# Kernel optimization log

Hardware: AMD Instinct MI355X
Metric: run time of the kernel (lower is better)

## Reference

```python
import jax, jax.numpy as jnp
import numpy as np
from jax import lax

D_MODEL = 1024
D_STATE = 128
D_CONV = 4
EXPAND = 2
HEADDIM = 64
D_INNER = EXPAND * D_MODEL          # 2048
NHEADS = D_INNER // HEADDIM         # 32
D_IN_PROJ = 2 * D_INNER + 2 * D_STATE + NHEADS  # 4384 (z, xBC, dt)
CONV_CH = D_INNER + 2 * D_STATE     # 2304
CHUNK = 128
EPS = 1e-5
BATCH, SEQ = 2, 2048


def silu(x):
    return x * jax.nn.sigmoid(x)


def rmsnorm(x, w):
    return x * lax.rsqrt(jnp.mean(x * x, axis=-1, keepdims=True) + EPS) * w


def segsum(a):
    # a: (b,h,c,q) -> (b,h,c,q,q); [i,j] = sum_{j<k<=i} a_k, -inf above diag
    q = a.shape[-1]
    cs = jnp.cumsum(a, axis=-1)
    seg = cs[..., :, None] - cs[..., None, :]
    mask = jnp.tril(jnp.ones((q, q), dtype=bool))
    return jnp.where(mask, seg, -jnp.inf)


def ssd(xh, dt, A, B, C):
    # xh: (b,l,h,p), dt: (b,l,h), A: (h,), B,C: (b,l,n). Chunked SSD scan.
    b, l, h, p = xh.shape
    n = B.shape[-1]
    c = l // CHUNK
    X = (xh * dt[..., None]).reshape(b, c, CHUNK, h, p)
    Adt = (A * dt).reshape(b, c, CHUNK, h).transpose(0, 3, 1, 2)  # (b,h,c,q)
    Bc = B.reshape(b, c, CHUNK, n)
    Cc = C.reshape(b, c, CHUNK, n)
    Acs = jnp.cumsum(Adt, axis=-1)
    L = jnp.exp(segsum(Adt))  # (b,h,c,q,q) causal decay within chunk
    Y_diag = jnp.einsum('bcln,bcsn,bhcls,bcshp->bclhp', Cc, Bc, L, X)
    decay_states = jnp.exp(Acs[..., -1:] - Acs)
    states = jnp.einsum('bcln,bhcl,bclhp->bchpn', Bc, decay_states, X)
    chunk_decay = jnp.exp(Acs[..., -1])  # (b,h,c)

    def step(s, inp):
        st, cd = inp
        return s * cd[:, :, None, None] + st, s

    init = jnp.zeros((b, h, p, n), dtype=xh.dtype)
    _, prev = lax.scan(step, init,
                       (states.transpose(1, 0, 2, 3, 4), chunk_decay.transpose(2, 0, 1)))
    # prev: (c,b,h,p,n) = state at start of each chunk
    Y_off = jnp.einsum('bcln,cbhpn,bhcl->bclhp', Cc, prev, jnp.exp(Acs))
    return (Y_diag + Y_off).reshape(b, l, h, p)


def mamba2(x, in_w, conv_w, conv_b, dt_bias, A_log, D, gnorm_w, out_w):
    b, l, _ = x.shape
    zxbcdt = x @ in_w.T  # (b,l,D_IN_PROJ)
    z = zxbcdt[..., :D_INNER]
    xBC = zxbcdt[..., D_INNER:D_INNER + CONV_CH]
    dt = jax.nn.softplus(zxbcdt[..., D_INNER + CONV_CH:] + dt_bias)  # (b,l,h)
    # causal depthwise conv1d
    xp = jnp.pad(xBC, ((0, 0), (D_CONV - 1, 0), (0, 0)))
    conv = sum(xp[:, k:k + l, :] * conv_w[:, k] for k in range(D_CONV)) + conv_b
    xBC = silu(conv)
    xs = xBC[..., :D_INNER]
    B = xBC[..., D_INNER:D_INNER + D_STATE]
    C = xBC[..., D_INNER + D_STATE:]
    A = -jnp.exp(A_log)
    xh = xs.reshape(b, l, NHEADS, HEADDIM)
    y = ssd(xh, dt, A, B, C) + xh * D[None, None, :, None]
    y = y.reshape(b, l, D_INNER)
    y = rmsnorm(y * silu(z), gnorm_w)  # RMSNormGated
    return y @ out_w.T


def setup_inputs() -> dict:
    key = jax.random.key(0)
    ks = jax.random.split(key, 24)
    d = {}
    d['x'] = jax.random.normal(ks[0], (BATCH, SEQ, D_MODEL), dtype=jnp.float32)
    d['norm_w'] = jnp.ones((D_MODEL,), jnp.float32)
    d['out_w_blk'] = jax.random.normal(ks[1], (D_MODEL, 2 * D_MODEL), jnp.float32) * 0.02
    d['out_b_blk'] = jnp.zeros((D_MODEL,), jnp.float32)
    for i, pfx in enumerate(['f_', 'b_']):
        o = 2 + i * 10
        d[pfx + 'in_w'] = jax.random.normal(ks[o], (D_IN_PROJ, D_MODEL), jnp.float32) * 0.02
        d[pfx + 'conv_w'] = jax.random.normal(ks[o + 1], (CONV_CH, D_CONV), jnp.float32) * 0.2
        d[pfx + 'conv_b'] = jnp.zeros((CONV_CH,), jnp.float32)
        d[pfx + 'dt_bias'] = jax.random.normal(ks[o + 2], (NHEADS,), jnp.float32) * 0.1
        d[pfx + 'A_log'] = jnp.log(jax.random.uniform(ks[o + 3], (NHEADS,), jnp.float32, 1.0, 16.0))
        d[pfx + 'D'] = jnp.ones((NHEADS,), jnp.float32)
        d[pfx + 'gnorm_w'] = jnp.ones((D_INNER,), jnp.float32)
        d[pfx + 'out_w'] = jax.random.normal(ks[o + 4], (D_MODEL, D_INNER), jnp.float32) * 0.02
    return d


def reference(x, norm_w, out_w_blk, out_b_blk,
              f_in_w, f_conv_w, f_conv_b, f_dt_bias, f_A_log, f_D, f_gnorm_w, f_out_w,
              b_in_w, b_conv_w, b_conv_b, b_dt_bias, b_A_log, b_D, b_gnorm_w, b_out_w):
    xn = rmsnorm(x, norm_w)
    y_fwd = mamba2(xn, f_in_w, f_conv_w, f_conv_b, f_dt_bias, f_A_log, f_D, f_gnorm_w, f_out_w)
    y_bwd = jnp.flip(
        mamba2(jnp.flip(xn, axis=1), b_in_w, b_conv_w, b_conv_b, b_dt_bias, b_A_log, b_D, b_gnorm_w, b_out_w),
        axis=1)
    out = jnp.concatenate([y_fwd, y_bwd], axis=-1) @ out_w_blk.T + out_b_blk
    return x + out
```

## Files before the change

kernel.cpp:

```cpp
#include <hip/hip_runtime.h>
#include <hip/hip_bf16.h>
#include <math.h>

#define BATCH 2
#define SEQL 2048
#define T 4096
#define DMODEL 1024
#define DINNER 2048
#define DSTATE 128
#define NH 32
#define HD 64
#define DPROJ2 4352
#define CONVCH 2304
#define NCH 16
#define CHUNK 128
#define EPS 1e-5f

#define N_INW ((size_t)DPROJ2 * DMODEL)
#define N_OUTW ((size_t)DMODEL * DINNER)
#define N_ST ((size_t)BATCH * NCH * NH * HD * DSTATE)
#define F2B_BLOCKS 10752
#define TW_BLOCKS 1024

typedef unsigned short u16;
typedef __bf16 bf16x8 __attribute__((ext_vector_type(8)));
typedef float f32x4 __attribute__((ext_vector_type(4)));

__device__ __forceinline__ u16 f2b(float f) {
    union { float f; unsigned u; } v; v.f = f;
    unsigned r = v.u + 0x7fffu + ((v.u >> 16) & 1u);
    return (u16)(r >> 16);
}
__device__ __forceinline__ float b2f(u16 b) {
    union { unsigned u; float f; } v; v.u = ((unsigned)b) << 16;
    return v.f;
}
__device__ __forceinline__ int flipseq(int r) {
    return (r & ~(SEQL - 1)) | ((SEQL - 1) - (r & (SEQL - 1)));
}
__device__ __forceinline__ void gload16(const u16* g, u16* l) {
    __builtin_amdgcn_global_load_lds(
        (const __attribute__((address_space(1))) void*)g,
        (__attribute__((address_space(3))) void*)l, 16, 0, 0);
}

#define FENCE asm volatile("" ::: "memory")

__device__ __forceinline__ float blockReduceSum(float v) {
    __shared__ float red_[4];
    for (int off = 32; off > 0; off >>= 1) v += __shfl_down(v, off);
    int lane = threadIdx.x & 63, wid = threadIdx.x >> 6;
    if (lane == 0) red_[wid] = v;
    __syncthreads();
    if (threadIdx.x == 0) {
        float s = 0.f;
        int nw = blockDim.x >> 6;
        for (int i = 0; i < nw; ++i) s += red_[i];
        red_[0] = s;
    }
    __syncthreads();
    return red_[0];
}

__global__ __launch_bounds__(256) void k_rmsdt(
    const float* __restrict__ x, const float* __restrict__ w,
    const float* __restrict__ inw_f, const float* __restrict__ inw_b,
    const float* __restrict__ dtb_f, const float* __restrict__ dtb_b,
    u16* __restrict__ outb, float* __restrict__ dt)
{
    __shared__ float xs[4][1024];
    int r0 = blockIdx.x * 4;
    int tid = threadIdx.x;
    int lane = tid & 63, wv = tid >> 6;
    int row = r0 + wv;
    const float* xr = x + (size_t)row * DMODEL;
    float4 v[4];
    float ss = 0.f;
    #pragma unroll
    for (int i = 0; i < 4; ++i) {
        v[i] = *(const float4*)(xr + (i * 64 + lane) * 4);
        ss += v[i].x * v[i].x + v[i].y * v[i].y + v[i].z * v[i].z + v[i].w * v[i].w;
    }
    #pragma unroll
    for (int off = 32; off > 0; off >>= 1) ss += __shfl_down(ss, off);
    ss = __shfl(ss, 0);
    float sc = rsqrtf(ss / DMODEL + EPS);
    #pragma unroll
    for (int i = 0; i < 4; ++i) {
        int c = (i * 64 + lane) * 4;
        float4 wv4 = *(const float4*)(w + c);
        ushort4 o;
        o.x = f2b(v[i].x * sc * wv4.x);
        o.y = f2b(v[i].y * sc * wv4.y);
        o.z = f2b(v[i].z * sc * wv4.z);
        o.w = f2b(v[i].w * sc * wv4.w);
        *(ushort4*)(outb + (size_t)row * DMODEL + c) = o;
        xs[wv][c + 0] = b2f(o.x); xs[wv][c + 1] = b2f(o.y);
        xs[wv][c + 2] = b2f(o.z); xs[wv][c + 3] = b2f(o.w);
    }
    __syncthreads();
    int h2 = tid >> 2, part = tid & 3;
    int dir = h2 >> 5, h = h2 & 31;
    const float* wd = (dir ? inw_b : inw_f) + (size_t)(DPROJ2 + h) * DMODEL;
    float a0 = 0.f, a1 = 0.f, a2 = 0.f, a3 = 0.f;
    for (int kk = 0; kk < 256; ++kk) {
        int k = part + (kk << 2);
        float wvv = wd[k];
        a0 += xs[0][k] * wvv; a1 += xs[1][k] * wvv;
        a2 += xs[2][k] * wvv; a3 += xs[3][k] * wvv;
    }
    #pragma unroll
    for (int off = 2; off > 0; off >>= 1) {
        a0 += __shfl_down(a0, off, 4); a1 += __shfl_down(a1, off, 4);
        a2 += __shfl_down(a2, off, 4); a3 += __shfl_down(a3, off, 4);
    }
    if (part == 0) {
        float bsh = dir ? dtb_b[h] : dtb_f[h];
        float* dtp = dt + (size_t)dir * T * NH;
        float vv[4] = {a0, a1, a2, a3};
        #pragma unroll
        for (int rr = 0; rr < 4; ++rr) {
            int rg = r0 + rr;
            if (dir) rg = flipseq(rg);
            float vvv = vv[rr] + bsh;
            dtp[(size_t)rg * NH + h] = (vvv > 20.f) ? vvv : log1pf(expf(vvv));
        }
    }
}

__global__ __launch_bounds__(256) void k_wprep(
    const float* __restrict__ f_in_w, const float* __restrict__ b_in_w,
    const float* __restrict__ out_w_blk,
    const float* __restrict__ f_out_w, const float* __restrict__ b_out_w,
    u16* __restrict__ d_inwb, u16* __restrict__ d_owbb, u16* __restrict__ d_fowT)
{
    __shared__ u16 t[64][65];
    int bid = blockIdx.x;
    if (bid < F2B_BLOCKS) {
        size_t i = ((size_t)bid * 256 + threadIdx.x) * 4;
        const float* s; u16* d; size_t off;
        if (i < 2 * N_INW) {
            int dir = i >= N_INW;
            off = i - (size_t)dir * N_INW;
            s = dir ? b_in_w : f_in_w; d = d_inwb + (size_t)dir * N_INW;
        } else {
            off = i - 2 * N_INW;
            if (off >= N_OUTW) return;
            s = out_w_blk; d = d_owbb;
        }
        float4 v = *(const float4*)(s + off);
        ushort4 o;
        o.x = f2b(v.x); o.y = f2b(v.y); o.z = f2b(v.z); o.w = f2b(v.w);
        *(ushort4*)(d + off) = o;
        return;
    }
    int b2 = bid - F2B_BLOCKS;
    int dir = b2 >> 9;
    int rem = b2 & 511;
    int c0 = (rem & 31) * 64, e0 = (rem >> 5) * 64;
    const float* src = dir ? b_out_w : f_out_w;
    u16* d = d_fowT + (size_t)dir * N_OUTW;
    for (int i = threadIdx.x; i < 64 * 16; i += 256) {
        int el = i >> 4, c4 = (i & 15) * 4;
        float4 v = *(const float4*)(src + (size_t)(e0 + el) * DINNER + c0 + c4);
        t[c4 + 0][el] = f2b(v.x); t[c4 + 1][el] = f2b(v.y);
        t[c4 + 2][el] = f2b(v.z); t[c4 + 3][el] = f2b(v.w);
    }
    __syncthreads();
    for (int i = threadIdx.x; i < 64 * 16; i += 256) {
        int cl = i >> 4, e4 = (i & 15) * 4;
        ushort4 o;
        o.x = t[cl][e4]; o.y = t[cl][e4 + 1]; o.z = t[cl][e4 + 2]; o.w = t[cl][e4 + 3];
        *(ushort4*)(d + (size_t)(c0 + cl) * DMODEL + e0 + e4) = o;
    }
}

__global__ __launch_bounds__(512, 2) void k_mm_in8(
    const u16* __restrict__ A, const u16* __restrict__ W0,
    u16* __restrict__ zb0, u16* __restrict__ xbcraw0)
{
    __shared__ u16 lds_[8 * 8192];
    int dir = blockIdx.z;
    const u16* W = W0 + (size_t)dir * N_INW;

    int f = blockIdx.x + (blockIdx.y << 4);
    int xcd = f & 7;
    int jj = f >> 3;
    int m0 = (jj >> 1) * 256;
    int n0 = ((xcd << 1) | (jj & 1)) * 256;

    u16* Cout; int ldcc, nbase;
    if (n0 < DINNER) {
        Cout = zb0 + (size_t)dir * T * DINNER;
        ldcc = DINNER;
        nbase = n0;
    } else {
        Cout = xbcraw0 + (size_t)dir * T * CONVCH;
        ldcc = CONVCH;
        nbase = n0 - DINNER;
    }

    int tid = threadIdx.x;
    int lane = tid & 63;
    int w = tid >> 6;
    int wm = w >> 2;
    int wn = w & 3;
    int l15 = lane & 15;
    int gsw0 = (((lane >> 4) ^ (lane & 7)) << 3);
    int gsw1 = (((4 + (lane >> 4)) ^ (lane & 7)) << 3);

    const u16* pA[2][2];
    const u16* pB[2][2];
    int swz = ((lane & 7) ^ (lane >> 3)) << 3;
    #pragma unroll
    for (int h = 0; h < 2; ++h)
        #pragma unroll
        for (int c = 0; c < 2; ++c) {
            int rl = (w * 2 + c) * 8 + (lane >> 3);
            int grow = m0 + h * 128 + rl;
            if (dir) grow = flipseq(grow);
            pA[h][c] = A + (size_t)grow * DMODEL + swz;
            pB[h][c] = W + (size_t)(n0 + h * 128 + rl) * DMODEL + swz;
        }
    int dst0 = (w * 2 + 0) * 512 + lane * 8;
    int dst1 = (w * 2 + 1) * 512 + lane * 8;

#define STAGE_A(t_, h_) do { \
        gload16(pA[h_][0] + (t_) * 64, lds_ + (((t_) & 1) * 4 + (h_)) * 8192 + dst0); \
        gload16(pA[h_][1] + (t_) * 64, lds_ + (((t_) & 1) * 4 + (h_)) * 8192 + dst1); \
    } while (0)
#define STAGE_B(t_, h_) do { \
        gload16(pB[h_][0] + (t_) * 64, lds_ + (((t_) & 1) * 4 + 2 + (h_)) * 8192 + dst0); \
        gload16(pB[h_][1] + (t_) * 64, lds_ + (((t_) & 1) * 4 + 2 + (h_)) * 8192 + dst1); \
    } while (0)

    f32x4 acc[8][4] = {};
    bf16x8 bfv[4][2];

    STAGE_A(0, 0); STAGE_A(0, 1); STAGE_B(0, 0); STAGE_B(0, 1);
    FENCE;
    STAGE_B(1, 0); STAGE_B(1, 1);
    asm volatile("s_waitcnt vmcnt(4)" ::: "memory");
    __builtin_amdgcn_s_barrier();
    FENCE;

    for (int kt = 0; kt < 16; ++kt) {
        int d = kt & 1;
        const u16* Ab = lds_ + (d * 4 + wm) * 8192;
        const u16* Bb = lds_ + (d * 4 + 2 + (wn >> 1)) * 8192;
        int nrow0 = (wn & 1) * 64;
        #pragma unroll
        for (int q = 0; q < 4; ++q) {
            if (q == 0) {
                #pragma unroll
                for (int j = 0; j < 4; ++j) {
                    const u16* bp = Bb + (nrow0 + j * 16 + l15) * 64;
                    bfv[j][0] = *(const bf16x8*)(bp + gsw0);
                    bfv[j][1] = *(const bf16x8*)(bp + gsw1);
                }
            }
            const u16* ap0 = Ab + ((q * 2 + 0) * 16 + l15) * 64;
            const u16* ap1 = Ab + ((q * 2 + 1) * 16 + l15) * 64;
            bf16x8 a0k0 = *(const bf16x8*)(ap0 + gsw0);
            bf16x8 a0k1 = *(const bf16x8*)(ap0 + gsw1);
            bf16x8 a1k0 = *(const bf16x8*)(ap1 + gsw0);
            bf16x8 a1k1 = *(const bf16x8*)(ap1 + gsw1);
            if (q == 0)      { if (kt < 15) STAGE_A(kt + 1, 0); }
            else if (q == 1) { if (kt < 15) STAGE_A(kt + 1, 1); }
            else if (q == 2) { if (kt < 14) STAGE_B(kt + 2, 0); }
            else             { if (kt < 14) STAGE_B(kt + 2, 1); }
            FENCE;
            __builtin_amdgcn_s_barrier();
            asm volatile("s_waitcnt lgkmcnt(0)" ::: "memory");
            __builtin_amdgcn_s_setprio(1);
            #pragma unroll
            for (int j = 0; j < 4; ++j) {
                acc[q * 2 + 0][j] = __builtin_amdgcn_mfma_f32_16x16x32_bf16(a0k0, bfv[j][0], acc[q * 2 + 0][j], 0, 0, 0);
                acc[q * 2 + 0][j] = __builtin_amdgcn_mfma_f32_16x16x32_bf16(a0k1, bfv[j][1], acc[q * 2 + 0][j], 0, 0, 0);
                acc[q * 2 + 1][j] = __builtin_amdgcn_mfma_f32_16x16x32_bf16(a1k0, bfv[j][0], acc[q * 2 + 1][j], 0, 0, 0);
                acc[q * 2 + 1][j] = __builtin_amdgcn_mfma_f32_16x16x32_bf16(a1k1, bfv[j][1], acc[q * 2 + 1][j], 0, 0, 0);
            }
            __builtin_amdgcn_s_setprio(0);
            if (q == 3) {
                if (kt < 14)       asm volatile("s_waitcnt vmcnt(4)" ::: "memory");
                else if (kt == 14) asm volatile("s_waitcnt vmcnt(0)" ::: "memory");
            }
            FENCE;
            __builtin_amdgcn_s_barrier();
            FENCE;
        }
    }
#undef STAGE_A
#undef STAGE_B

    int rb = m0 + wm * 128 + ((lane >> 4) << 2);
    int cb = nbase + wn * 64 + l15;
    #pragma unroll
    for (int i = 0; i < 8; ++i)
        #pragma unroll
        for (int j = 0; j < 4; ++j)
            #pragma unroll
            for (int r = 0; r < 4; ++r)
                Cout[(size_t)(rb + i * 16 + r) * ldcc + cb + j * 16] = f2b(acc[i][j][r]);
}

__global__ __launch_bounds__(256, 4) void k_mm_in(
    const u16* __restrict__ A, const u16* __restrict__ W0,
    u16* __restrict__ zb0, u16* __restrict__ xbcraw0, int ny0)
{
    const int K = DMODEL;
    int dir = blockIdx.z;
    const u16* W = W0 + (size_t)dir * N_INW;
    int m0 = blockIdx.x * 128, n0 = (blockIdx.y + ny0) * 128;

    u16* Cout;
    int ldcc, nbase;
    if (n0 < DINNER) {
        Cout = zb0 + (size_t)dir * T * DINNER;
        ldcc = DINNER;
        nbase = n0;
    } else {
        Cout = xbcraw0 + (size_t)dir * T * CONVCH;
        ldcc = CONVCH;
        nbase = n0 - DINNER;
    }

    __shared__ u16 As[2 * 128 * 32];
    __shared__ u16 Bs[2 * 128 * 32];
    int tid = threadIdx.x;
    int lane = tid & 63;
    int wrow = ((tid >> 6) & 1) * 64, wcol = (tid >> 7) * 64;

    int srow = tid >> 2, skof = (tid & 3) * 8;
    int ar1 = m0 + srow, ar2 = ar1 + 64;
    if (dir) { ar1 = flipseq(ar1); ar2 = flipseq(ar2); }
    const u16* ga1 = A + (size_t)ar1 * K + skof;
    const u16* ga2 = A + (size_t)ar2 * K + skof;
    const u16* gb1 = W + (size_t)(n0 + srow) * K + skof;
    const u16* gb2 = gb1 + (size_t)64 * K;
    u16* la1 = As + tid * 8;
    u16* la2 = As + 2048 + tid * 8;
    u16* lb1 = Bs + tid * 8;
    u16* lb2 = Bs + 2048 + tid * 8;

    int aoff[4], boff[4];
    #pragma unroll
    for (int i = 0; i < 4; ++i) {
        aoff[i] = (wrow + i * 16 + (lane & 15)) * 32 + ((lane >> 4) * 8);
        boff[i] = (wcol + i * 16 + (lane & 15)) * 32 + ((lane >> 4) * 8);
    }

    f32x4 acc[4][4] = {};
    for (int kt = 0; kt < K; kt += 64) {
        gload16(ga1, la1);        gload16(ga2, la2);
        gload16(ga1 + 32, la1 + 4096); gload16(ga2 + 32, la2 + 4096);
        gload16(gb1, lb1);        gload16(gb2, lb2);
        gload16(gb1 + 32, lb1 + 4096); gload16(gb2 + 32, lb2 + 4096);
        ga1 += 64; ga2 += 64; gb1 += 64; gb2 += 64;
        __syncthreads();
        #pragma unroll
        for (int ks = 0; ks < 2; ++ks) {
            bf16x8 af[4], bfv[4];
            #pragma unroll
            for (int i = 0; i < 4; ++i) af[i] = *(const bf16x8*)(As + ks * 4096 + aoff[i]);
            #pragma unroll
            for (int j = 0; j < 4; ++j) bfv[j] = *(const bf16x8*)(Bs + ks * 4096 + boff[j]);
            #pragma unroll
            for (int i = 0; i < 4; ++i)
                #pragma unroll
                for (int j = 0; j < 4; ++j)
                    acc[i][j] = __builtin_amdgcn_mfma_f32_16x16x32_bf16(af[i], bfv[j], acc[i][j], 0, 0, 0);
        }
        __syncthreads();
    }

    int rbase = m0 + wrow + ((lane >> 4) << 2);
    int cbase = nbase + wcol + (lane & 15);
    #pragma unroll
    for (int i = 0; i < 4; ++i)
        #pragma unroll
        for (int j = 0; j < 4; ++j)
            #pragma unroll
            for (int r = 0; r < 4; ++r)
                Cout[(size_t)(rbase + i * 16 + r) * ldcc + cbase + j * 16] = f2b(acc[i][j][r]);
}

__global__ __launch_bounds__(256) void k_mm64(
    const u16* __restrict__ A0, const u16* __restrict__ W0,
    u16* __restrict__ Cb)
{
    int dir = blockIdx.z;
    const u16* A = A0 + dir * DMODEL;
    const u16* W = W0 + (size_t)dir * N_OUTW;

    __shared__ u16 As[2 * 128 * 32];
    __shared__ u16 Bs[2 * 64 * 32];
    int tid = threadIdx.x;
    int lane = tid & 63;
    int w = tid >> 6;
    int m0 = blockIdx.y * 128, n0 = blockIdx.x * 64;
    int wrow = (w & 1) * 64, wcol = (w >> 1) * 32;

    int srow = tid >> 2, skof = (tid & 3) * 8;
    const u16* ga1 = A + (size_t)(m0 + srow) * 2048 + skof;
    const u16* ga2 = A + (size_t)(m0 + 64 + srow) * 2048 + skof;
    const u16* gb  = W + (size_t)(n0 + srow) * DMODEL + skof;
    u16* la1 = As + tid * 8;
    u16* la2 = As + 2048 + tid * 8;
    u16* lb  = Bs + tid * 8;

    int aoff[4], boff[2];
    #pragma unroll
    for (int i = 0; i < 4; ++i)
        aoff[i] = (wrow + i * 16 + (lane & 15)) * 32 + ((lane >> 4) * 8);
    #pragma unroll
    for (int j = 0; j < 2; ++j)
        boff[j] = (wcol + j * 16 + (lane & 15)) * 32 + ((lane >> 4) * 8);

    f32x4 acc[4][2] = {};
    for (int kt = 0; kt < DMODEL; kt += 64) {
        gload16(ga1, la1); gload16(ga1 + 32, la1 + 4096);
        gload16(ga2, la2); gload16(ga2 + 32, la2 + 4096);
        gload16(gb, lb);   gload16(gb + 32, lb + 2048);
        ga1 += 64; ga2 += 64; gb += 64;
        __syncthreads();
        #pragma unroll
        for (int ks = 0; ks < 2; ++ks) {
            bf16x8 af[4], bfv[2];
            #pragma unroll
            for (int i = 0; i < 4; ++i) af[i] = *(const bf16x8*)(As + ks * 4096 + aoff[i]);
            #pragma unroll
            for (int j = 0; j < 2; ++j) bfv[j] = *(const bf16x8*)(Bs + ks * 2048 + boff[j]);
            #pragma unroll
            for (int i = 0; i < 4; ++i)
                #pragma unroll
                for (int j = 0; j < 2; ++j)
                    acc[i][j] = __builtin_amdgcn_mfma_f32_16x16x32_bf16(af[i], bfv[j], acc[i][j], 0, 0, 0);
        }
        __syncthreads();
    }

    int rbase = m0 + wrow + ((lane >> 4) << 2);
    int cbase = n0 + wcol + (lane & 15);
    #pragma unroll
    for (int i = 0; i < 4; ++i)
        #pragma unroll
        for (int j = 0; j < 2; ++j)
            #pragma unroll
            for (int r = 0; r < 4; ++r)
                Cb[(size_t)(rbase + i * 16 + r) * 4096 + dir * 2048 + cbase + j * 16] = f2b(acc[i][j][r]);
}

__global__ __launch_bounds__(256) void k_mm_fin(
    const u16* __restrict__ A1, const u16* __restrict__ A2,
    const u16* __restrict__ W,
    float* __restrict__ out, const float* __restrict__ bias,
    const float* __restrict__ resid)
{
    __shared__ u16 As[4 * 128 * 32];
    __shared__ u16 Bs[2 * 2 * 64 * 32];
    int tid = threadIdx.x;
    int lane = tid & 63;
    int w = tid >> 6;
    int m0 = blockIdx.y * 128, n0 = blockIdx.x * 64;
    int wrow = (w & 1) * 64, wcol = (w >> 1) * 32;

    int srow = tid >> 2, skof = (tid & 3) * 8;
    const u16* ga1  = A1 + (size_t)(m0 + srow) * DINNER + skof;
    const u16* ga1b = A1 + (size_t)(m0 + 64 + srow) * DINNER + skof;
    const u16* ga2  = A2 + (size_t)flipseq(m0 + srow) * DINNER + skof;
    const u16* ga2b = A2 + (size_t)flipseq(m0 + 64 + srow) * DINNER + skof;
    const u16* gb1 = W + (size_t)(n0 + srow) * 4096 + skof;
    const u16* gb2 = gb1 + 2048;
    u16* la1  = As + tid * 8;
    u16* la1b = As + 2048 + tid * 8;
    u16* la2  = As + 8192 + tid * 8;
    u16* la2b = As + 8192 + 2048 + tid * 8;
    u16* lb1 = Bs + tid * 8;
    u16* lb2 = Bs + 4096 + tid * 8;

    int aoff[4], boff[2];
    #pragma unroll
    for (int i = 0; i < 4; ++i)
        aoff[i] = (wrow + i * 16 + (lane & 15)) * 32 + ((lane >> 4) * 8);
    #pragma unroll
    for (int j = 0; j < 2; ++j)
        boff[j] = (wcol + j * 16 + (lane & 15)) * 32 + ((lane >> 4) * 8);

    f32x4 acc[4][2] = {};
    for (int kt = 0; kt < DINNER; kt += 64) {
        gload16(ga1, la1);    gload16(ga1 + 32, la1 + 4096);
        gload16(ga1b, la1b);  gload16(ga1b + 32, la1b + 4096);
        gload16(ga2, la2);    gload16(ga2 + 32, la2 + 4096);
        gload16(ga2b, la2b);  gload16(ga2b + 32, la2b + 4096);
        gload16(gb1, lb1);    gload16(gb1 + 32, lb1 + 2048);
        gload16(gb2, lb2);    gload16(gb2 + 32, lb2 + 2048);
        ga1 += 64; ga1b += 64; ga2 += 64; ga2b += 64; gb1 += 64; gb2 += 64;
        __syncthreads();
        #pragma unroll
        for (int h = 0; h < 2; ++h) {
            #pragma unroll
            for (int ks = 0; ks < 2; ++ks) {
                bf16x8 af[4], bfv[2];
                #pragma unroll
                for (int i = 0; i < 4; ++i)
                    af[i] = *(const bf16x8*)(As + h * 8192 + ks * 4096 + aoff[i]);
                #pragma unroll
                for (int j = 0; j < 2; ++j)
                    bfv[j] = *(const bf16x8*)(Bs + h * 4096 + ks * 2048 + boff[j]);
                #pragma unroll
                for (int i = 0; i < 4; ++i)
                    #pragma unroll
                    for (int j = 0; j < 2; ++j)
                        acc[i][j] = __builtin_amdgcn_mfma_f32_16x16x32_bf16(af[i], bfv[j], acc[i][j], 0, 0, 0);
            }
        }
        __syncthreads();
    }

    int rbase = m0 + wrow + ((lane >> 4) << 2);
    int cbase = n0 + wcol + (lane & 15);
    #pragma unroll
    for (int i = 0; i < 4; ++i)
        #pragma unroll
        for (int j = 0; j < 2; ++j)
            #pragma unroll
            for (int r = 0; r < 4; ++r) {
                int row = rbase + i * 16 + r, col = cbase + j * 16;
                out[(size_t)row * DMODEL + col] =
                    acc[i][j][r] + bias[col] + resid[(size_t)row * DMODEL + col];
            }
}

__global__ void k_conv(const u16* __restrict__ xraw0,
                       const float* __restrict__ cw_f, const float* __restrict__ cw_b,
                       const float* __restrict__ cb_f, const float* __restrict__ cb_b,
                       const float* __restrict__ dt0,
                       u16* __restrict__ xbcb0, u16* __restrict__ xdtb0)
{
    int dir = blockIdx.z;
    const u16* xraw = xraw0 + (size_t)dir * T * CONVCH;
    const float* cw = dir ? cw_b : cw_f;
    const float* cb = dir ? cb_b : cb_f;
    const float* dt = dt0 + (size_t)dir * T * NH;
    u16* xbcb = xbcb0 + (size_t)dir * T * CONVCH;
    u16* xdtb = xdtb0 + (size_t)dir * T * DINNER;

    int idx = blockIdx.x * blockDim.x + threadIdx.x;
    if (idx >= (T / 4) * (CONVCH / 8)) return;
    int r4 = idx / (CONVCH / 8);
    int c8 = (idx - r4 * (CONVCH / 8)) * 8;
    int r0 = r4 * 4;
    int t0 = r0 & (SEQL - 1);

    float4 cwv[8];
    #pragma unroll
    for (int j = 0; j < 8; ++j) cwv[j] = *(const float4*)(cw + (size_t)(c8 + j) * 4);
    float acc[4][8];
    {
        float4 c0 = *(const float4*)(cb + c8);
        float4 c1 = *(const float4*)(cb + c8 + 4);
        #pragma unroll
        for (int i = 0; i < 4; ++i) {
            acc[i][0] = c0.x; acc[i][1] = c0.y; acc[i][2] = c0.z; acc[i][3] = c0.w;
            acc[i][4] = c1.x; acc[i][5] = c1.y; acc[i][6] = c1.z; acc[i][7] = c1.w;
        }
    }
    #pragma unroll
    for (int s = 0; s < 7; ++s) {
        int tt = t0 - 3 + s;
        if (tt < 0) continue;
        const u16* src = xraw + (size_t)(r0 - 3 + s) * CONVCH + c8;
        ushort4 v0 = *(const ushort4*)src;
        ushort4 v1 = *(const ushort4*)(src + 4);
        float xv[8] = {b2f(v0.x), b2f(v0.y), b2f(v0.z), b2f(v0.w),
                       b2f(v1.x), b2f(v1.y), b2f(v1.z), b2f(v1.w)};
        #pragma unroll
        for (int i = 0; i < 4; ++i) {
            if (i <= s && i >= s - 3) {
                const int j = s - i;
                #pragma unroll
                for (int ch = 0; ch < 8; ++ch) {
                    float wv = (j == 0) ? cwv[ch].x : (j == 1) ? cwv[ch].y
                             : (j == 2) ? cwv[ch].z : cwv[ch].w;
                    acc[i][ch] += xv[ch] * wv;
                }
            }
        }
    }
    #pragma unroll
    for (int i = 0; i < 4; ++i) {
        int r = r0 + i;
        float sgl[8];
        #pragma unroll
        for (int ch = 0; ch < 8; ++ch) sgl[ch] = acc[i][ch] / (1.f + __expf(-acc[i][ch]));
        ushort4 o0, o1;
        o0.x = f2b(sgl[0]); o0.y = f2b(sgl[1]); o0.z = f2b(sgl[2]); o0.w = f2b(sgl[3]);
        o1.x = f2b(sgl[4]); o1.y = f2b(sgl[5]); o1.z = f2b(sgl[6]); o1.w = f2b(sgl[7]);
        *(ushort4*)(xbcb + (size_t)r * CONVCH + c8) = o0;
        *(ushort4*)(xbcb + (size_t)r * CONVCH + c8 + 4) = o1;
        if (c8 < DINNER) {
            float dv = dt[(size_t)r * NH + (c8 >> 6)];
            ushort4 d0, d1;
            d0.x = f2b(sgl[0] * dv); d0.y = f2b(sgl[1] * dv);
            d0.z = f2b(sgl[2] * dv); d0.w = f2b(sgl[3] * dv);
            d1.x = f2b(sgl[4] * dv); d1.y = f2b(sgl[5] * dv);
            d1.z = f2b(sgl[6] * dv); d1.w = f2b(sgl[7] * dv);
            *(ushort4*)(xdtb + (size_t)r * DINNER + c8) = d0;
            *(ushort4*)(xdtb + (size_t)r * DINNER + c8 + 4) = d1;
        }
    }
}

#define LDW 136
__global__ __launch_bounds__(256) void k_states(
    const u16* __restrict__ xbcb0, const u16* __restrict__ xdtb0,
    const float* __restrict__ dt0,
// ... 164 lines not shown
    for (int i = 0; i < 4; ++i)
        #pragma unroll
        for (int j = 0; j < 4; ++j) {
            int s = wcol + j * 16 + (lane & 15);
            #pragma unroll
            for (int r = 0; r < 4; ++r) {
                int l = wrow + i * 16 + (lane >> 4) * 4 + r;
                float v = (s <= l) ? sacc[i][j][r] * __expf(acs_s[l] - acs_s[s]) : 0.f;
                S0[l * LDW + s] = f2b(v);
            }
        }
    __syncthreads();
    f32x4 yacc[2][4] = {};
    for (int kk = 0; kk < 4; ++kk) {
        bf16x8 af[2], bfr[4];
        #pragma unroll
        for (int i = 0; i < 2; ++i)
            af[i] = *(const bf16x8*)(S0 + (w * 32 + i * 16 + (lane & 15)) * LDW
                                     + kk * 32 + (lane >> 4) * 8);
        #pragma unroll
        for (int j = 0; j < 4; ++j)
            bfr[j] = *(const bf16x8*)(Xt + (j * 16 + (lane & 15)) * LDW
                                      + kk * 32 + (lane >> 4) * 8);
        #pragma unroll
        for (int i = 0; i < 2; ++i)
            #pragma unroll
            for (int j = 0; j < 4; ++j)
                yacc[i][j] = __builtin_amdgcn_mfma_f32_16x16x32_bf16(af[i], bfr[j], yacc[i][j], 0, 0, 0);
    }
    __syncthreads();
    size_t sb = (size_t)blockIdx.x * (HD * DSTATE);
    for (int i = tid; i < 64 * 16; i += 256) {
        int p = i >> 4, m8 = (i & 15) * 8;
        *(uint4*)(S0 + p * LDW + m8) = *(const uint4*)(prev + sb + (size_t)p * DSTATE + m8);
    }
    __syncthreads();
    f32x4 oacc[2][4] = {};
    for (int kk = 0; kk < 4; ++kk) {
        bf16x8 af[2], bfr[4];
        #pragma unroll
        for (int i = 0; i < 2; ++i)
            af[i] = *(const bf16x8*)(cbase + (size_t)(w * 32 + i * 16 + (lane & 15)) * CONVCH
                                     + kk * 32 + (lane >> 4) * 8);
        #pragma unroll
        for (int j = 0; j < 4; ++j)
            bfr[j] = *(const bf16x8*)(S0 + (j * 16 + (lane & 15)) * LDW
                                      + kk * 32 + (lane >> 4) * 8);
        #pragma unroll
        for (int i = 0; i < 2; ++i)
            #pragma unroll
            for (int j = 0; j < 4; ++j)
                oacc[i][j] = __builtin_amdgcn_mfma_f32_16x16x32_bf16(af[i], bfr[j], oacc[i][j], 0, 0, 0);
    }
    float Dh = Dp[h];
    #pragma unroll
    for (int i = 0; i < 2; ++i)
        #pragma unroll
        for (int j = 0; j < 4; ++j)
            #pragma unroll
            for (int r = 0; r < 4; ++r) {
                int l = w * 32 + i * 16 + (lane >> 4) * 4 + r;
                int p = j * 16 + (lane & 15);
                float val = yacc[i][j][r] + __expf(acs_s[l]) * oacc[i][j][r]
                          + b2f(xbcb[(size_t)(row0 + l) * CONVCH + h * HD + p]) * Dh;
                y[(size_t)(row0 + l) * DINNER + h * HD + p] = f2b(val);
            }
}

__global__ __launch_bounds__(256) void k_gate(
    const u16* __restrict__ y0, const u16* __restrict__ zb0,
    const float* __restrict__ gw_f, const float* __restrict__ gw_b,
    u16* __restrict__ out0)
{
    int dir = blockIdx.z;
    const u16* y = y0 + (size_t)dir * T * DINNER;
    const u16* zb = zb0 + (size_t)dir * T * DINNER;
    const float* gw = dir ? gw_b : gw_f;
    u16* out = out0 + (size_t)dir * T * DINNER;

    int r = blockIdx.x;
    int tid = threadIdx.x;
    float tv[8];
    float ss = 0.f;
    #pragma unroll
    for (int it = 0; it < 2; ++it) {
        int i = (it * 256 + tid) * 4;
        ushort4 yv = *(const ushort4*)(y + (size_t)r * DINNER + i);
        ushort4 zv = *(const ushort4*)(zb + (size_t)r * DINNER + i);
        float z0 = b2f(zv.x), z1 = b2f(zv.y), z2 = b2f(zv.z), z3 = b2f(zv.w);
        float t0 = b2f(yv.x) * (z0 / (1.f + __expf(-z0)));
        float t1 = b2f(yv.y) * (z1 / (1.f + __expf(-z1)));
        float t2 = b2f(yv.z) * (z2 / (1.f + __expf(-z2)));
        float t3 = b2f(yv.w) * (z3 / (1.f + __expf(-z3)));
        tv[it * 4 + 0] = t0; tv[it * 4 + 1] = t1; tv[it * 4 + 2] = t2; tv[it * 4 + 3] = t3;
        ss += t0 * t0 + t1 * t1 + t2 * t2 + t3 * t3;
    }
    float tot = blockReduceSum(ss);
    float sc = rsqrtf(tot / DINNER + EPS);
    #pragma unroll
    for (int it = 0; it < 2; ++it) {
        int i = (it * 256 + tid) * 4;
        ushort4 o;
        o.x = f2b(tv[it * 4 + 0] * sc * gw[i]);
        o.y = f2b(tv[it * 4 + 1] * sc * gw[i + 1]);
        o.z = f2b(tv[it * 4 + 2] * sc * gw[i + 2]);
        o.w = f2b(tv[it * 4 + 3] * sc * gw[i + 3]);
        *(ushort4*)(out + (size_t)r * DINNER + i) = o;
    }
}

extern "C" void kernel_launch(void* const* d_in, const int* in_sizes, int n_in,
                              void* d_out, int out_size, void* d_ws, size_t ws_size,
                              hipStream_t stream)
{
    const float* x         = (const float*)d_in[0];
    const float* norm_w    = (const float*)d_in[1];
    const float* out_w_blk = (const float*)d_in[2];
    const float* out_b_blk = (const float*)d_in[3];
    const float* f_in_w    = (const float*)d_in[4];
    const float* f_conv_w  = (const float*)d_in[5];
    const float* f_conv_b  = (const float*)d_in[6];
    const float* f_dt_bias = (const float*)d_in[7];
    const float* f_A_log   = (const float*)d_in[8];
    const float* f_D       = (const float*)d_in[9];
    const float* f_gnorm_w = (const float*)d_in[10];
    const float* f_out_w   = (const float*)d_in[11];
    const float* b_in_w    = (const float*)d_in[12];
    const float* b_conv_w  = (const float*)d_in[13];
    const float* b_conv_b  = (const float*)d_in[14];
    const float* b_dt_bias = (const float*)d_in[15];
    const float* b_A_log   = (const float*)d_in[16];
    const float* b_D       = (const float*)d_in[17];
    const float* b_gnorm_w = (const float*)d_in[18];
    const float* b_out_w   = (const float*)d_in[19];
    float* out = (float*)d_out;

    char* ws = (char*)d_ws;
    u16*  xnb    = (u16*)ws;   ws += (size_t)T * DMODEL * 2;
    u16*  zb     = (u16*)ws;   ws += (size_t)2 * T * DINNER * 2;
    u16*  xbcraw = (u16*)ws;   ws += (size_t)2 * T * CONVCH * 2;
    u16*  xbcb   = (u16*)ws;   ws += (size_t)2 * T * CONVCH * 2;
    u16*  xdtb   = (u16*)ws;   ws += (size_t)2 * T * DINNER * 2;
    float* dtb   = (float*)ws; ws += (size_t)2 * T * NH * 4;
    float* acs   = (float*)ws; ws += (size_t)2 * BATCH * NH * NCH * CHUNK * 4;
    float* cd    = (float*)ws; ws += (size_t)2 * BATCH * NH * NCH * 4;
    u16*  stb    = (u16*)ws;   ws += (size_t)2 * N_ST * 2;
    u16*  inwb   = (u16*)ws;   ws += (size_t)2 * N_INW * 2;
    u16*  fowT2  = (u16*)ws;   ws += (size_t)2 * N_OUTW * 2;
    u16*  owbb   = (u16*)ws;   ws += (size_t)N_OUTW * 2;
    u16*  yb16  = xbcraw;
    u16*  ybb   = xdtb;
    u16*  Mcomb = xbcb;

    k_rmsdt<<<T / 4, 256, 0, stream>>>(x, norm_w, f_in_w, b_in_w,
                                       f_dt_bias, b_dt_bias, xnb, dtb);
    k_wprep<<<F2B_BLOCKS + TW_BLOCKS, 256, 0, stream>>>(
        f_in_w, b_in_w, out_w_blk, f_out_w, b_out_w, inwb, owbb, fowT2);

    {
        dim3 g(T / 256, 16, 2);
        k_mm_in8<<<g, 512, 0, stream>>>(xnb, inwb, zb, xbcraw);
    }
    {
        dim3 g(T / 128, 2, 2);
        k_mm_in<<<g, 256, 0, stream>>>(xnb, inwb, zb, xbcraw, 32);
    }
    {
        dim3 g(((T / 4) * (CONVCH / 8) + 255) / 256, 1, 2);
        k_conv<<<g, 256, 0, stream>>>(xbcraw, f_conv_w, b_conv_w, f_conv_b, b_conv_b,
                                      dtb, xbcb, xdtb);
    }
    {
        dim3 g(BATCH * NCH * NH, 1, 2);
        k_states<<<g, 256, 0, stream>>>(xbcb, xdtb, dtb, f_A_log, b_A_log, acs, cd, stb);
    }
    k_scan<<<(2 * BATCH * NH * HD * DSTATE) / 256, 256, 0, stream>>>(stb, cd);
    {
        dim3 g(BATCH * NCH * NH, 1, 2);
        k_chunk<<<g, 256, 0, stream>>>(xbcb, xdtb, acs, stb, f_D, b_D, yb16);
    }
    {
        dim3 g(T, 1, 2);
        k_gate<<<g, 256, 0, stream>>>(yb16, zb, f_gnorm_w, b_gnorm_w, ybb);
    }
    {
        dim3 g(DINNER / 64, DMODEL / 128, 2);
        k_mm64<<<g, 256, 0, stream>>>(owbb, fowT2, Mcomb);
    }
    {
        dim3 g(DMODEL / 64, T / 128, 1);
        k_mm_fin<<<g, 256, 0, stream>>>(ybb, ybb + (size_t)T * DINNER, Mcomb,
                                        out, out_b_blk, x);
    }
}
```

Measured before the change: 507.3 us.

## Merge prep kernels and input GEMM tail into single launches with XCD-aware block mapping

```diff
diff --git a/kernel.cpp b/kernel.cpp
--- a/kernel.cpp
+++ b/kernel.cpp
@@ -62,82 +62,81 @@
     return red_[0];
 }
 
-__global__ __launch_bounds__(256) void k_rmsdt(
+__global__ __launch_bounds__(256) void k_prep(
     const float* __restrict__ x, const float* __restrict__ w,
-    const float* __restrict__ inw_f, const float* __restrict__ inw_b,
+    const float* __restrict__ f_in_w, const float* __restrict__ b_in_w,
     const float* __restrict__ dtb_f, const float* __restrict__ dtb_b,
-    u16* __restrict__ outb, float* __restrict__ dt)
-{
-    __shared__ float xs[4][1024];
-    int r0 = blockIdx.x * 4;
-    int tid = threadIdx.x;
-    int lane = tid & 63, wv = tid >> 6;
-    int row = r0 + wv;
-    const float* xr = x + (size_t)row * DMODEL;
-    float4 v[4];
-    float ss = 0.f;
-    #pragma unroll
-    for (int i = 0; i < 4; ++i) {
-        v[i] = *(const float4*)(xr + (i * 64 + lane) * 4);
-        ss += v[i].x * v[i].x + v[i].y * v[i].y + v[i].z * v[i].z + v[i].w * v[i].w;
-    }
-    #pragma unroll
-    for (int off = 32; off > 0; off >>= 1) ss += __shfl_down(ss, off);
-    ss = __shfl(ss, 0);
-    float sc = rsqrtf(ss / DMODEL + EPS);
-    #pragma unroll
-    for (int i = 0; i < 4; ++i) {
-        int c = (i * 64 + lane) * 4;
-        float4 wv4 = *(const float4*)(w + c);
-        ushort4 o;
-        o.x = f2b(v[i].x * sc * wv4.x);
-        o.y = f2b(v[i].y * sc * wv4.y);
-        o.z = f2b(v[i].z * sc * wv4.z);
-        o.w = f2b(v[i].w * sc * wv4.w);
-        *(ushort4*)(outb + (size_t)row * DMODEL + c) = o;
-        xs[wv][c + 0] = b2f(o.x); xs[wv][c + 1] = b2f(o.y);
-        xs[wv][c + 2] = b2f(o.z); xs[wv][c + 3] = b2f(o.w);
-    }
-    __syncthreads();
-    int h2 = tid >> 2, part = tid & 3;
-    int dir = h2 >> 5, h = h2 & 31;
-    const float* wd = (dir ? inw_b : inw_f) + (size_t)(DPROJ2 + h) * DMODEL;
-    float a0 = 0.f, a1 = 0.f, a2 = 0.f, a3 = 0.f;
-    for (int kk = 0; kk < 256; ++kk) {
-        int k = part + (kk << 2);
-        float wvv = wd[k];
-        a0 += xs[0][k] * wvv; a1 += xs[1][k] * wvv;
-        a2 += xs[2][k] * wvv; a3 += xs[3][k] * wvv;
-    }
-    #pragma unroll
-    for (int off = 2; off > 0; off >>= 1) {
-        a0 += __shfl_down(a0, off, 4); a1 += __shfl_down(a1, off, 4);
-        a2 += __shfl_down(a2, off, 4); a3 += __shfl_down(a3, off, 4);
-    }
-    if (part == 0) {
-        float bsh = dir ? dtb_b[h] : dtb_f[h];
-        float* dtp = dt + (size_t)dir * T * NH;
-        float vv[4] = {a0, a1, a2, a3};
-        #pragma unroll
-        for (int rr = 0; rr < 4; ++rr) {
-            int rg = r0 + rr;
-            if (dir) rg = flipseq(rg);
-            float vvv = vv[rr] + bsh;
-            dtp[(size_t)rg * NH + h] = (vvv > 20.f) ? vvv : log1pf(expf(vvv));
-        }
-    }
-}
-
-__global__ __launch_bounds__(256) void k_wprep(
-    const float* __restrict__ f_in_w, const float* __restrict__ b_in_w,
+    u16* __restrict__ outb, float* __restrict__ dt,
     const float* __restrict__ out_w_blk,
     const float* __restrict__ f_out_w, const float* __restrict__ b_out_w,
     u16* __restrict__ d_inwb, u16* __restrict__ d_owbb, u16* __restrict__ d_fowT)
 {
+    __shared__ float xs[4][1024];
     __shared__ u16 t[64][65];
-    int bid = blockIdx.x;
+    int bid0 = blockIdx.x;
+    int tid = threadIdx.x;
+    if (bid0 < 1024) {
+        int r0 = bid0 * 4;
+        int lane = tid & 63, wv = tid >> 6;
+        int row = r0 + wv;
+        const float* xr = x + (size_t)row * DMODEL;
+        float4 v[4];
+        float ss = 0.f;
+        #pragma unroll
+        for (int i = 0; i < 4; ++i) {
+            v[i] = *(const float4*)(xr + (i * 64 + lane) * 4);
+            ss += v[i].x * v[i].x + v[i].y * v[i].y + v[i].z * v[i].z + v[i].w * v[i].w;
+        }
+        #pragma unroll
+        for (int off = 32; off > 0; off >>= 1) ss += __shfl_down(ss, off);
+        ss = __shfl(ss, 0);
+        float sc = rsqrtf(ss / DMODEL + EPS);
+        #pragma unroll
+        for (int i = 0; i < 4; ++i) {
+            int c = (i * 64 + lane) * 4;
+            float4 wv4 = *(const float4*)(w + c);
+            ushort4 o;
+            o.x = f2b(v[i].x * sc * wv4.x);
+            o.y = f2b(v[i].y * sc * wv4.y);
+            o.z = f2b(v[i].z * sc * wv4.z);
+            o.w = f2b(v[i].w * sc * wv4.w);
+            *(ushort4*)(outb + (size_t)row * DMODEL + c) = o;
+            xs[wv][c + 0] = b2f(o.x); xs[wv][c + 1] = b2f(o.y);
+            xs[wv][c + 2] = b2f(o.z); xs[wv][c + 3] = b2f(o.w);
+        }
+        __syncthreads();
+        int h2 = tid >> 2, part = tid & 3;
+        int dir = h2 >> 5, h = h2 & 31;
+        const float* wd = (dir ? b_in_w : f_in_w) + (size_t)(DPROJ2 + h) * DMODEL;
+        float a0 = 0.f, a1 = 0.f, a2 = 0.f, a3 = 0.f;
+        for (int kk = 0; kk < 256; ++kk) {
+            int k = part + (kk << 2);
+            float wvv = wd[k];
+            a0 += xs[0][k] * wvv; a1 += xs[1][k] * wvv;
+            a2 += xs[2][k] * wvv; a3 += xs[3][k] * wvv;
+        }
+        #pragma unroll
+        for (int off = 2; off > 0; off >>= 1) {
+            a0 += __shfl_down(a0, off, 4); a1 += __shfl_down(a1, off, 4);
+            a2 += __shfl_down(a2, off, 4); a3 += __shfl_down(a3, off, 4);
+        }
+        if (part == 0) {
+            float bsh = dir ? dtb_b[h] : dtb_f[h];
+            float* dtp = dt + (size_t)dir * T * NH;
+            float vv[4] = {a0, a1, a2, a3};
+            #pragma unroll
+            for (int rr = 0; rr < 4; ++rr) {
+                int rg = r0 + rr;
+                if (dir) rg = flipseq(rg);
+                float vvv = vv[rr] + bsh;
+                dtp[(size_t)rg * NH + h] = (vvv > 20.f) ? vvv : log1pf(expf(vvv));
+            }
+        }
+        return;
+    }
+    int bid = bid0 - 1024;
     if (bid < F2B_BLOCKS) {
-        size_t i = ((size_t)bid * 256 + threadIdx.x) * 4;
+        size_t i = ((size_t)bid * 256 + tid) * 4;
         const float* s; u16* d; size_t off;
         if (i < 2 * N_INW) {
             int dir = i >= N_INW;
@@ -160,14 +159,14 @@
     int c0 = (rem & 31) * 64, e0 = (rem >> 5) * 64;
     const float* src = dir ? b_out_w : f_out_w;
     u16* d = d_fowT + (size_t)dir * N_OUTW;
-    for (int i = threadIdx.x; i < 64 * 16; i += 256) {
+    for (int i = tid; i < 64 * 16; i += 256) {
         int el = i >> 4, c4 = (i & 15) * 4;
         float4 v = *(const float4*)(src + (size_t)(e0 + el) * DINNER + c0 + c4);
         t[c4 + 0][el] = f2b(v.x); t[c4 + 1][el] = f2b(v.y);
         t[c4 + 2][el] = f2b(v.z); t[c4 + 3][el] = f2b(v.w);
     }
     __syncthreads();
-    for (int i = threadIdx.x; i < 64 * 16; i += 256) {
+    for (int i = tid; i < 64 * 16; i += 256) {
         int cl = i >> 4, e4 = (i & 15) * 4;
         ushort4 o;
         o.x = t[cl][e4]; o.y = t[cl][e4 + 1]; o.z = t[cl][e4 + 2]; o.w = t[cl][e4 + 3];
@@ -175,15 +174,82 @@
     }
 }
 
-__global__ __launch_bounds__(512, 2) void k_mm_in8(
+__global__ __launch_bounds__(512, 2) void k_mm_inx(
     const u16* __restrict__ A, const u16* __restrict__ W0,
     u16* __restrict__ zb0, u16* __restrict__ xbcraw0)
 {
     __shared__ u16 lds_[8 * 8192];
-    int dir = blockIdx.z;
+    int bid = blockIdx.x;
+    int tid = threadIdx.x;
+    int lane = tid & 63;
+    int w = tid >> 6;
+    int l15 = lane & 15;
+
+    if (bid >= 512) {
+        int c = bid - 512;
+        int dirc = c >> 6;
+        int cc = c & 63;
+        int m0 = (cc & 31) * 128;
+        int n0 = (32 + (cc >> 5)) * 128;
+        const u16* W = W0 + (size_t)dirc * N_INW;
+        u16* Cout = xbcraw0 + (size_t)dirc * T * CONVCH;
+        int nbase = n0 - DINNER;
+
+        u16* As = lds_;
+        u16* Bs = lds_ + 8192;
+        int srow = tid >> 2, skof = (tid & 3) * 8;
+        int ar = m0 + srow;
+        if (dirc) ar = flipseq(ar);
+        const u16* ga = A + (size_t)ar * DMODEL + skof;
+        const u16* gb = W + (size_t)(n0 + srow) * DMODEL + skof;
+        u16* la = As + tid * 8;
+        u16* lb = Bs + tid * 8;
+
+        int wrow = (w & 1) * 64, wcol = (w >> 1) * 32;
+        int aoff[4], boff[2];
+        #pragma unroll
+        for (int i = 0; i < 4; ++i)
+            aoff[i] = (wrow + i * 16 + l15) * 32 + ((lane >> 4) * 8);
+        #pragma unroll
+        for (int j = 0; j < 2; ++j)
+            boff[j] = (wcol + j * 16 + l15) * 32 + ((lane >> 4) * 8);
+
+        f32x4 acc[4][2] = {};
+        for (int kt = 0; kt < DMODEL; kt += 64) {
+            gload16(ga, la);      gload16(ga + 32, la + 4096);
+            gload16(gb, lb);      gload16(gb + 32, lb + 4096);
+            ga += 64; gb += 64;
+            __syncthreads();
+            #pragma unroll
+            for (int ks = 0; ks < 2; ++ks) {
+                bf16x8 af[4], bfv[2];
+                #pragma unroll
+                for (int i = 0; i < 4; ++i) af[i] = *(const bf16x8*)(As + ks * 4096 + aoff[i]);
+                #pragma unroll
+                for (int j = 0; j < 2; ++j) bfv[j] = *(const bf16x8*)(Bs + ks * 4096 + boff[j]);
+                #pragma unroll
+                for (int i = 0; i < 4; ++i)
+                    #pragma unroll
+                    for (int j = 0; j < 2; ++j)
+                        acc[i][j] = __builtin_amdgcn_mfma_f32_16x16x32_bf16(af[i], bfv[j], acc[i][j], 0, 0, 0);
+            }
+            __syncthreads();
+        }
+        int rbase = m0 + wrow + ((lane >> 4) << 2);
+        int cbase = nbase + wcol + l15;
+        #pragma unroll
+        for (int i = 0; i < 4; ++i)
+            #pragma unroll
+            for (int j = 0; j < 2; ++j)
+                #pragma unroll
+                for (int r = 0; r < 4; ++r)
+                    Cout[(size_t)(rbase + i * 16 + r) * CONVCH + cbase + j * 16] = f2b(acc[i][j][r]);
+        return;
+    }
+
+    int dir = bid >> 8;
     const u16* W = W0 + (size_t)dir * N_INW;
-
-    int f = blockIdx.x + (blockIdx.y << 4);
+    int f = bid & 255;
     int xcd = f & 7;
     int jj = f >> 3;
     int m0 = (jj >> 1) * 256;
@@ -200,12 +266,8 @@
         nbase = n0 - DINNER;
     }
 
-    int tid = threadIdx.x;
-    int lane = tid & 63;
-    int w = tid >> 6;
     int wm = w >> 2;
     int wn = w & 3;
-    int l15 = lane & 15;
     int gsw0 = (((lane >> 4) ^ (lane & 7)) << 3);
     int gsw1 = (((4 + (lane >> 4)) ^ (lane & 7)) << 3);
 
@@ -304,92 +366,16 @@
                 Cout[(size_t)(rb + i * 16 + r) * ldcc + cb + j * 16] = f2b(acc[i][j][r]);
 }
 
-__global__ __launch_bounds__(256, 4) void k_mm_in(
-    const u16* __restrict__ A, const u16* __restrict__ W0,
-    u16* __restrict__ zb0, u16* __restrict__ xbcraw0, int ny0)
-{
-    const int K = DMODEL;
-    int dir = blockIdx.z;
-    const u16* W = W0 + (size_t)dir * N_INW;
-    int m0 = blockIdx.x * 128, n0 = (blockIdx.y + ny0) * 128;
-
-    u16* Cout;
-    int ldcc, nbase;
-    if (n0 < DINNER) {
-        Cout = zb0 + (size_t)dir * T * DINNER;
-        ldcc = DINNER;
-        nbase = n0;
-    } else {
-        Cout = xbcraw0 + (size_t)dir * T * CONVCH;
-        ldcc = CONVCH;
-        nbase = n0 - DINNER;
-    }
-
-    __shared__ u16 As[2 * 128 * 32];
-    __shared__ u16 Bs[2 * 128 * 32];
-    int tid = threadIdx.x;
-    int lane = tid & 63;
-    int wrow = ((tid >> 6) & 1) * 64, wcol = (tid >> 7) * 64;
-
-    int srow = tid >> 2, skof = (tid & 3) * 8;
-    int ar1 = m0 + srow, ar2 = ar1 + 64;
-    if (dir) { ar1 = flipseq(ar1); ar2 = flipseq(ar2); }
-    const u16* ga1 = A + (size_t)ar1 * K + skof;
-    const u16* ga2 = A + (size_t)ar2 * K + skof;
-    const u16* gb1 = W + (size_t)(n0 + srow) * K + skof;
-    const u16* gb2 = gb1 + (size_t)64 * K;
-    u16* la1 = As + tid * 8;
-    u16* la2 = As + 2048 + tid * 8;
-    u16* lb1 = Bs + tid * 8;
-    u16* lb2 = Bs + 2048 + tid * 8;
-
-    int aoff[4], boff[4];
-    #pragma unroll
-    for (int i = 0; i < 4; ++i) {
-        aoff[i] = (wrow + i * 16 + (lane & 15)) * 32 + ((lane >> 4) * 8);
-        boff[i] = (wcol + i * 16 + (lane & 15)) * 32 + ((lane >> 4) * 8);
-    }
-
-    f32x4 acc[4][4] = {};
-    for (int kt = 0; kt < K; kt += 64) {
-        gload16(ga1, la1);        gload16(ga2, la2);
-        gload16(ga1 + 32, la1 + 4096); gload16(ga2 + 32, la2 + 4096);
-        gload16(gb1, lb1);        gload16(gb2, lb2);
-        gload16(gb1 + 32, lb1 + 4096); gload16(gb2 + 32, lb2 + 4096);
-        ga1 += 64; ga2 += 64; gb1 += 64; gb2 += 64;
-        __syncthreads();
-        #pragma unroll
-        for (int ks = 0; ks < 2; ++ks) {
-            bf16x8 af[4], bfv[4];
-            #pragma unroll
-            for (int i = 0; i < 4; ++i) af[i] = *(const bf16x8*)(As + ks * 4096 + aoff[i]);
-            #pragma unroll
-            for (int j = 0; j < 4; ++j) bfv[j] = *(const bf16x8*)(Bs + ks * 4096 + boff[j]);
-            #pragma unroll
-            for (int i = 0; i < 4; ++i)
-                #pragma unroll
-                for (int j = 0; j < 4; ++j)
-                    acc[i][j] = __builtin_amdgcn_mfma_f32_16x16x32_bf16(af[i], bfv[j], acc[i][j], 0, 0, 0);
-        }
-        __syncthreads();
-    }
-
-    int rbase = m0 + wrow + ((lane >> 4) << 2);
-    int cbase = nbase + wcol + (lane & 15);
-    #pragma unroll
-    for (int i = 0; i < 4; ++i)
-        #pragma unroll
-        for (int j = 0; j < 4; ++j)
-            #pragma unroll
-            for (int r = 0; r < 4; ++r)
-                Cout[(size_t)(rbase + i * 16 + r) * ldcc + cbase + j * 16] = f2b(acc[i][j][r]);
-}
-
 __global__ __launch_bounds__(256) void k_mm64(
     const u16* __restrict__ A0, const u16* __restrict__ W0,
     u16* __restrict__ Cb)
 {
-    int dir = blockIdx.z;
+    int bid = blockIdx.x;
+    int xcd = bid & 7;
+    int j9 = bid >> 3;
+    int dir = j9 >> 5;
+    int m0 = xcd * 128;
+    int n0 = (j9 & 31) * 64;
     const u16* A = A0 + dir * DMODEL;
     const u16* W = W0 + (size_t)dir * N_OUTW;
 
@@ -398,7 +384,6 @@
     int tid = threadIdx.x;
     int lane = tid & 63;
     int w = tid >> 6;
-    int m0 = blockIdx.y * 128, n0 = blockIdx.x * 64;
     int wrow = (w & 1) * 64, wcol = (w >> 1) * 32;
 
     int srow = tid >> 2, skof = (tid & 3) * 8;
@@ -459,10 +444,14 @@
 {
     __shared__ u16 As[4 * 128 * 32];
     __shared__ u16 Bs[2 * 2 * 64 * 32];
+    int bid = blockIdx.x;
+    int xcd = bid & 7;
+    int j9 = bid >> 3;
+    int m0 = (xcd * 4 + (j9 & 3)) * 128;
+    int n0 = (j9 >> 2) * 64;
     int tid = threadIdx.x;
     int lane = tid & 63;
     int w = tid >> 6;
-    int m0 = blockIdx.y * 128, n0 = blockIdx.x * 64;
     int wrow = (w & 1) * 64, wcol = (w >> 1) * 32;
 
     int srow = tid >> 2, skof = (tid & 3) * 8;
@@ -933,19 +922,12 @@
     u16*  ybb   = xdtb;
     u16*  Mcomb = xbcb;
 
-    k_rmsdt<<<T / 4, 256, 0, stream>>>(x, norm_w, f_in_w, b_in_w,
-                                       f_dt_bias, b_dt_bias, xnb, dtb);
-    k_wprep<<<F2B_BLOCKS + TW_BLOCKS, 256, 0, stream>>>(
-        f_in_w, b_in_w, out_w_blk, f_out_w, b_out_w, inwb, owbb, fowT2);
-
-    {
-        dim3 g(T / 256, 16, 2);
-        k_mm_in8<<<g, 512, 0, stream>>>(xnb, inwb, zb, xbcraw);
-    }
-    {
-        dim3 g(T / 128, 2, 2);
-        k_mm_in<<<g, 256, 0, stream>>>(xnb, inwb, zb, xbcraw, 32);
-    }
+    k_prep<<<1024 + F2B_BLOCKS + TW_BLOCKS, 256, 0, stream>>>(
+        x, norm_w, f_in_w, b_in_w, f_dt_bias, b_dt_bias, xnb, dtb,
+        out_w_blk, f_out_w, b_out_w, inwb, owbb, fowT2);
+
+    k_mm_inx<<<640, 512, 0, stream>>>(xnb, inwb, zb, xbcraw);
+
     {
         dim3 g(((T / 4) * (CONVCH / 8) + 255) / 256, 1, 2);
         k_conv<<<g, 256, 0, stream>>>(xbcraw, f_conv_w, b_conv_w, f_conv_b, b_conv_b,
@@ -964,13 +946,7 @@
         dim3 g(T, 1, 2);
         k_gate<<<g, 256, 0, stream>>>(yb16, zb, f_gnorm_w, b_gnorm_w, ybb);
     }
-    {
-        dim3 g(DINNER / 64, DMODEL / 128, 2);
-        k_mm64<<<g, 256, 0, stream>>>(owbb, fowT2, Mcomb);
-    }
-    {
-        dim3 g(DMODEL / 64, T / 128, 1);
-        k_mm_fin<<<g, 256, 0, stream>>>(ybb, ybb + (size_t)T * DINNER, Mcomb,
-                                        out, out_b_blk, x);
-    }
-}
+    k_mm64<<<512, 256, 0, stream>>>(owbb, fowT2, Mcomb);
+    k_mm_fin<<<512, 256, 0, stream>>>(ybb, ybb + (size_t)T * DINNER, Mcomb,
+                                      out, out_b_blk, x);
+}
```

Result: faster. 491.9 us (-3.0%).
